# Optimization experiments

Hardware: AMD Instinct MI355X
Metric: run time of the kernel (lower is better)

## Reference

```python
import jax, jax.numpy as jnp
import numpy as np

EPSILON = 0.1
ALPHA = 0.5
N_ITER = 10
B, N, D, N_USERS = 4096, 4096, 16, 100000


def setup_inputs() -> dict:
    key = jax.random.key(0)
    k1, k2, k3, k4, k5, k6 = jax.random.split(key, 6)
    users_tensor = jax.random.randint(k1, (B,), 0, N_USERS)
    pois_tensor = jax.random.randint(k2, (B, N), 0, N)
    D_tensor = jax.random.uniform(k3, (B, N), dtype=jnp.float32)
    # ScaledEmbedding: normal init scaled by 1/embedding_dim
    poi_emb = jax.random.normal(k4, (N, D), dtype=jnp.float32) / D
    user_emb = jax.random.normal(k5, (N_USERS, D), dtype=jnp.float32) / D
    capacities = jax.random.uniform(k6, (N,), dtype=jnp.float32) + 0.5
    return {"users_tensor": users_tensor, "pois_tensor": pois_tensor,
            "D_tensor": D_tensor, "poi_emb": poi_emb,
            "user_emb": user_emb, "capacities": capacities}


def reference(users_tensor, pois_tensor, D_tensor, poi_emb, user_emb, capacities):
    pe = poi_emb[pois_tensor]            # [B, N, D]
    ue = user_emb[users_tensor]          # [B, D]
    dot = jnp.einsum('bnd,bd->bn', pe, ue)   # [B, N]
    affinity = (1.0 - ALPHA) * dot - ALPHA * (D_tensor / jnp.mean(D_tensor))
    K = jnp.exp(affinity / EPSILON)      # [B, N]
    a = jnp.ones((B,), dtype=K.dtype)
    b = capacities

    def body(i, uv):
        u, v = uv
        u = a / (K @ v)        # [B]
        v = b / (K.T @ u)      # [N]
        return (u, v)

    u0 = jnp.ones((B,), dtype=K.dtype)
    v0 = jnp.ones((N,), dtype=K.dtype)
    u, v = jax.lax.fori_loop(0, N_ITER, body, (u0, v0))
    P = K * (u[:, None] * v[None, :])    # [B, N]
    return P
```

## Files before the change

### kernel.cpp

```cpp
#include <hip/hip_runtime.h>
#include <hip/hip_fp16.h>

#define BB 4096
#define NN 4096
#define RPB 4
#define RPI 16
#define IBLK (BB / RPI)
#define NSL IBLK
#define RPP 8
#define NTSLOT 60

__device__ __forceinline__ int swzK(int bid) { return (bid & 7) * 128 + (bid >> 3); }

typedef float vf4 __attribute__((ext_vector_type(4)));
typedef float vf2 __attribute__((ext_vector_type(2)));
typedef int   vi4 __attribute__((ext_vector_type(4)));
typedef float fv2 __attribute__((ext_vector_type(2)));
__device__ __forceinline__ float4 ntl4(const float4* p) {
    vf4 r = __builtin_nontemporal_load((const vf4*)p);
    return *(float4*)&r;
}
__device__ __forceinline__ int4 ntl4i(const int4* p) {
    vi4 r = __builtin_nontemporal_load((const vi4*)p);
    return *(int4*)&r;
}
__device__ __forceinline__ void nts4(float4* p, float4 v) {
    __builtin_nontemporal_store(*(vf4*)&v, (vf4*)p);
}
__device__ __forceinline__ void nts2(float2* p, float2 v) {
    __builtin_nontemporal_store(*(vf2*)&v, (vf2*)p);
}

__device__ __forceinline__ void dec4(int w, float* f) {
    fv2 lo = __builtin_amdgcn_cvt_pk_f32_fp8(w, false);
    fv2 hi = __builtin_amdgcn_cvt_pk_f32_fp8(w, true);
    f[0] = lo.x; f[1] = lo.y; f[2] = hi.x; f[3] = hi.y;
}

__global__ __launch_bounds__(256) void k_mean(
        const float* __restrict__ Dt, float* __restrict__ dsum,
        float* __restrict__ v) {
    const int tid = blockIdx.x * blockDim.x + threadIdx.x;
    const int gs = gridDim.x * blockDim.x;
    if (tid < NN) v[tid] = 1.0f;
    const float4* D4 = (const float4*)Dt;
    const int total4 = (BB * NN) / 4;
    float s = 0.f;
    for (int i = tid; i < total4; i += gs) {
        float4 d = ntl4(&D4[i]);
        s += (d.x + d.y) + (d.z + d.w);
    }
    #pragma unroll
    for (int off = 32; off > 0; off >>= 1) s += __shfl_down(s, off, 64);
    __shared__ float ls[4];
    if ((threadIdx.x & 63) == 0) ls[threadIdx.x >> 6] = s;
    __syncthreads();
    if (threadIdx.x == 0) atomicAdd(dsum, (ls[0] + ls[1]) + (ls[2] + ls[3]));
}

__global__ __launch_bounds__(256) void k_K(
        const int* __restrict__ users, const int* __restrict__ pois,
        const float* __restrict__ Dt, const float* __restrict__ poi_emb,
        const float* __restrict__ user_emb, const float* __restrict__ dsum,
        __half* __restrict__ K, unsigned char* __restrict__ K8) {
    __shared__ __half slut[RPB][NN];
    __shared__ float ues[RPB * 16];
    const int t = threadIdx.x;
    const int b0 = swzK(blockIdx.x) * RPB;
    if (t < RPB * 16) {
        int r = t >> 4, d = t & 15;
        ues[t] = user_emb[(size_t)users[b0 + r] * 16 + d];
    }
    __syncthreads();
    float ue[RPB][16];
    #pragma unroll
    for (int r = 0; r < RPB; r++)
        #pragma unroll
        for (int d = 0; d < 16; d++) ue[r][d] = ues[r * 16 + d];

    const float4* pe4 = (const float4*)poi_emb;
    for (int j = t; j < NN; j += 256) {
        float4 p0 = pe4[j * 4 + 0];
        float4 p1 = pe4[j * 4 + 1];
        float4 p2 = pe4[j * 4 + 2];
        float4 p3 = pe4[j * 4 + 3];
        #pragma unroll
        for (int r = 0; r < RPB; r++) {
            float acc = p0.x*ue[r][0]  + p0.y*ue[r][1]  + p0.z*ue[r][2]  + p0.w*ue[r][3]
                      + p1.x*ue[r][4]  + p1.y*ue[r][5]  + p1.z*ue[r][6]  + p1.w*ue[r][7]
                      + p2.x*ue[r][8]  + p2.y*ue[r][9]  + p2.z*ue[r][10] + p2.w*ue[r][11]
                      + p3.x*ue[r][12] + p3.y*ue[r][13] + p3.z*ue[r][14] + p3.w*ue[r][15];
            slut[r][j] = __float2half(acc);
        }
    }
    __syncthreads();
    const float cc = 5.0f * 16777216.0f / dsum[0];
    #pragma unroll
    for (int r = 0; r < RPB; r++) {
        const size_t base = (size_t)(b0 + r) * NN;
        const int4*   p4 = (const int4*)(pois + base);
        const float4* d4 = (const float4*)(Dt + base);
        #pragma unroll
        for (int i = 0; i < NN / 4 / 256; i++) {
            const int q = t + i * 256;
            int4   ci = ntl4i(&p4[q]);
            float4 cd = ntl4(&d4[q]);
            float k0 = __expf(5.0f * __half2float(slut[r][ci.x]) - cc * cd.x);
            float k1 = __expf(5.0f * __half2float(slut[r][ci.y]) - cc * cd.y);
            float k2 = __expf(5.0f * __half2float(slut[r][ci.z]) - cc * cd.z);
            float k3 = __expf(5.0f * __half2float(slut[r][ci.w]) - cc * cd.w);
            __half2 ha = __floats2half2_rn(k0, k1);
            __half2 hb = __floats2half2_rn(k2, k3);
            float2 w16;
            *(__half2*)&w16.x = ha;
            *(__half2*)&w16.y = hb;
            nts2((float2*)&K[base + 4 * (size_t)q], w16);
            int w8 = __builtin_amdgcn_cvt_pk_fp8_f32(16.f * k0, 16.f * k1, 0, false);
            w8 = __builtin_amdgcn_cvt_pk_fp8_f32(16.f * k2, 16.f * k3, w8, true);
            __builtin_nontemporal_store(w8, &((int*)(K8 + base))[q]);
        }
    }
}

__global__ __launch_bounds__(1024) void k_it(
        const unsigned char* __restrict__ K8, const float* __restrict__ v,
        float* __restrict__ part, float* __restrict__ u) {
    const int t = threadIdx.x;
    const int c = t & 511;
    const int rh = t >> 9;
    const int sb = (blockIdx.x & 7) * 32 + (blockIdx.x >> 3);
    const int r0 = sb * RPI + rh * 8;

    const float4* w4 = (const float4*)v;
    float4 w0 = w4[2 * c], w1 = w4[2 * c + 1];

    uint2 h8[8];
    #pragma unroll
    for (int r = 0; r < 8; r++)
        h8[r] = ((const uint2*)(K8 + (size_t)(r0 + r) * NN))[c];

    float acc[8];
    #pragma unroll
    for (int r = 0; r < 8; r++) {
        float f[8];
        dec4((int)h8[r].x, f);
        dec4((int)h8[r].y, f + 4);
        acc[r] = f[0]*w0.x + f[1]*w0.y + f[2]*w0.z + f[3]*w0.w
               + f[4]*w1.x + f[5]*w1.y + f[6]*w1.z + f[7]*w1.w;
    }
    #pragma unroll
    for (int off = 32; off > 0; off >>= 1)
        #pragma unroll
        for (int r = 0; r < 8; r++) acc[r] += __shfl_down(acc[r], off, 64);
    __shared__ float ls[16][8];
    __shared__ float us[16];
    if ((t & 63) == 0)
        #pragma unroll
        for (int r = 0; r < 8; r++) ls[t >> 6][r] = acc[r];
    __syncthreads();
    if (t < 16) {
        const int wb = (t < 8) ? 0 : 8;
        const int rr = (t < 8) ? t : (t - 8);
        float s = 0.f;
        #pragma unroll
        for (int wv = 0; wv < 8; wv++) s += ls[wb + wv][rr];
        float uu = 1.0f / s;
        us[t] = uu;
        u[sb * RPI + t] = 16.0f * uu;
    }
    __syncthreads();

    float4 A0 = make_float4(0, 0, 0, 0), A1 = A0;
    #pragma unroll
    for (int r = 0; r < 8; r++) {
        const float ur = us[rh * 8 + r];
        float f[8];
        dec4((int)h8[r].x, f);
        dec4((int)h8[r].y, f + 4);
        A0.x += ur * f[0]; A0.y += ur * f[1]; A0.z += ur * f[2]; A0.w += ur * f[3];
        A1.x += ur * f[4]; A1.y += ur * f[5]; A1.z += ur * f[6]; A1.w += ur * f[7];
    }
    __shared__ float4 ps[512][2];
    if (rh == 1) { ps[c][0] = A0; ps[c][1] = A1; }
    __syncthreads();
    if (rh == 0) {
        float4 B0 = ps[c][0], B1 = ps[c][1];
        A0.x += B0.x; A0.y += B0.y; A0.z += B0.z; A0.w += B0.w;
        A1.x += B1.x; A1.y += B1.y; A1.z += B1.z; A1.w += B1.w;
        float4* p4 = (float4*)(part + (size_t)sb * NN);
        nts4(&p4[2 * c],     A0);
        nts4(&p4[2 * c + 1], A1);
    }
}

__global__ __launch_bounds__(256) void k_red(
        const float* __restrict__ part, const float* __restrict__ cap,
        float* __restrict__ v) {
    const int t = threadIdx.x;
    const int g = blockIdx.x;
    const int j = t & 7;
    const int s = t >> 3;
    const float4* p4 = (const float4*)part;
    float4 a = make_float4(0, 0, 0, 0);
    #pragma unroll
    for (int i = 0; i < NSL / 32; i++) {
        float4 x = ntl4(&p4[(size_t)(s + 32 * i) * (NN / 4) + g * 8 + j]);
        a.x += x.x; a.y += x.y; a.z += x.z; a.w += x.w;
    }
    __shared__ float4 red[32][8];
    red[s][j] = a;
    __syncthreads();
    if (t < 8) {
        float4 b = red[0][t];
        #pragma unroll
        for (int s2 = 1; s2 < 32; s2++) {
            float4 x = red[s2][t];
            b.x += x.x; b.y += x.y; b.z += x.z; b.w += x.w;
        }
        float4 cc = ((const float4*)cap)[g * 8 + t];
        ((float4*)v)[g * 8 + t] =
            make_float4(cc.x / b.x, cc.y / b.y, cc.z / b.z, cc.w / b.w);
    }
}

__global__ __launch_bounds__(256) void k_P(
        const __half* __restrict__ K, const float* __restrict__ u,
        const float* __restrict__ v, float* __restrict__ P) {
    const int t = threadIdx.x;
    const int slot = blockIdx.x >> 3;
    const int sb = (blockIdx.x & 7) * 64 + slot;
    const int r0 = sb * RPP;
    const bool nt = (slot >= NTSLOT);
    const float4* v4 = (const float4*)v;
    float4 va0 = v4[2 * t],       va1 = v4[2 * t + 1];
    float4 vb0 = v4[512 + 2 * t], vb1 = v4[512 + 2 * t + 1];
    #pragma unroll 2
    for (int r = 0; r < RPP; r++) {
        const int b = r0 + r;
        const float ub = u[b];
        const size_t base = (size_t)b * NN;
        const float4* k4 = (const float4*)(K + base);
        float4 raw0 = nt ? ntl4(&k4[t])       : k4[t];
        float4 raw1 = nt ? ntl4(&k4[256 + t]) : k4[256 + t];
        const __half2* ha = (const __half2*)&raw0;
        const __half2* hb = (const __half2*)&raw1;
        float2 f0 = __half22float2(ha[0]);
        float2 f1 = __half22float2(ha[1]);
        float2 f2 = __half22float2(ha[2]);
        float2 f3 = __half22float2(ha[3]);
        float2 g0 = __half22float2(hb[0]);
        float2 g1 = __half22float2(hb[1]);
        float2 g2 = __half22float2(hb[2]);
        float2 g3 = __half22float2(hb[3]);
        float4* P4 = (float4*)(P + base);
        nts4(&P4[2*t],       make_float4(f0.x*ub*va0.x, f0.y*ub*va0.y, f1.x*ub*va0.z, f1.y*ub*va0.w));
        nts4(&P4[2*t+1],     make_float4(f2.x*ub*va1.x, f2.y*ub*va1.y, f3.x*ub*va1.z, f3.y*ub*va1.w));
        nts4(&P4[512+2*t],   make_float4(g0.x*ub*vb0.x, g0.y*ub*vb0.y, g1.x*ub*vb0.z, g1.y*ub*vb0.w));
        nts4(&P4[512+2*t+1], make_float4(g2.x*ub*vb1.x, g2.y*ub*vb1.y, g3.x*ub*vb1.z, g3.y*ub*vb1.w));
    }
}

extern "C" void kernel_launch(void* const* d_in, const int* in_sizes, int n_in,
                              void* d_out, int out_size, void* d_ws, size_t ws_size,
                              hipStream_t stream) {
    const int*   users    = (const int*)d_in[0];
    const int*   pois     = (const int*)d_in[1];
    const float* Dt       = (const float*)d_in[2];
    const float* poi_emb  = (const float*)d_in[3];
    const float* user_emb = (const float*)d_in[4];
    const float* cap      = (const float*)d_in[5];
    float* out = (float*)d_out;

    float*  wsf  = (float*)d_ws;
    float*  dsum = wsf;
    float*  u    = wsf + 64;
    float*  v    = wsf + 64 + BB;
    __half* Kh   = (__half*)(wsf + 64 + BB + NN);
    float*  part = (float*)d_out;
    unsigned char* K8 = (unsigned char*)(part + (size_t)NSL * NN);

    (void)hipMemsetAsync(dsum, 0, sizeof(float), stream);
    k_mean<<<2048, 256, 0, stream>>>(Dt, dsum, v);
    k_K<<<BB / RPB, 256, 0, stream>>>(users, pois, Dt, poi_emb, user_emb, dsum, Kh, K8);
    for (int it = 0; it < 10; it++) {
        k_it<<<IBLK, 1024, 0, stream>>>(K8, v, part, u);
        k_red<<<128, 256, 0, stream>>>(part, cap, v);
    }
    k_P<<<BB / RPP, 256, 0, stream>>>(Kh, u, v, out);
}
```

Baseline: 358.4 us.

## Fuse Sinkhorn iteration and column reduction into one kernel with counter-based grid sync

Merges the per-iteration row-scaling/partial-sum kernel and the column-reduction kernel into a single launch. Extra reducer blocks spin on per-iteration atomic counters until every producer block has published its partial column sums, then compute v. Producers publish those partials with agent-scope atomic stores. This removes one kernel launch and its boundary per iteration, ten in total. The cost is spin-waiting reducer blocks and a reliance on producer blocks being scheduled before the reducers.

```diff
diff --git a/kernel.cpp b/kernel.cpp
--- a/kernel.cpp
+++ b/kernel.cpp
@@ -5,10 +5,11 @@
 #define NN 4096
 #define RPB 4
 #define RPI 16
-#define IBLK (BB / RPI)
-#define NSL IBLK
+#define NSL 256
+#define NRED 64
 #define RPP 8
 #define NTSLOT 60
+#define CNT_INTS (10 * 8 * 16)
 
 __device__ __forceinline__ int swzK(int bid) { return (bid & 7) * 128 + (bid >> 3); }
 
@@ -37,12 +38,24 @@
     f[0] = lo.x; f[1] = lo.y; f[2] = hi.x; f[3] = hi.y;
 }
 
+__device__ __forceinline__ void ast8(unsigned long long* p, float a, float b) {
+    union { float2 f; unsigned long long q; } u;
+    u.f = make_float2(a, b);
+    __hip_atomic_store(p, u.q, __ATOMIC_RELAXED, __HIP_MEMORY_SCOPE_AGENT);
+}
+__device__ __forceinline__ float2 ald8(const unsigned long long* p) {
+    union { float2 f; unsigned long long q; } u;
+    u.q = __hip_atomic_load(p, __ATOMIC_RELAXED, __HIP_MEMORY_SCOPE_AGENT);
+    return u.f;
+}
+
 __global__ __launch_bounds__(256) void k_mean(
         const float* __restrict__ Dt, float* __restrict__ dsum,
-        float* __restrict__ v) {
+        float* __restrict__ v, int* __restrict__ cnt) {
     const int tid = blockIdx.x * blockDim.x + threadIdx.x;
     const int gs = gridDim.x * blockDim.x;
     if (tid < NN) v[tid] = 1.0f;
+    if (tid < CNT_INTS) cnt[tid] = 0;
     const float4* D4 = (const float4*)Dt;
     const int total4 = (BB * NN) / 4;
     float s = 0.f;
@@ -122,104 +135,123 @@
     }
 }
 
-__global__ __launch_bounds__(1024) void k_it(
-        const unsigned char* __restrict__ K8, const float* __restrict__ v,
-        float* __restrict__ part, float* __restrict__ u) {
+__global__ __launch_bounds__(1024) void k_itf(
+        const unsigned char* __restrict__ K8, float* __restrict__ v,
+        float* __restrict__ part, float* __restrict__ u,
+        const float* __restrict__ cap, int* __restrict__ cnt) {
     const int t = threadIdx.x;
-    const int c = t & 511;
-    const int rh = t >> 9;
-    const int sb = (blockIdx.x & 7) * 32 + (blockIdx.x >> 3);
-    const int r0 = sb * RPI + rh * 8;
-
-    const float4* w4 = (const float4*)v;
-    float4 w0 = w4[2 * c], w1 = w4[2 * c + 1];
-
-    uint2 h8[8];
-    #pragma unroll
-    for (int r = 0; r < 8; r++)
-        h8[r] = ((const uint2*)(K8 + (size_t)(r0 + r) * NN))[c];
-
-    float acc[8];
-    #pragma unroll
-    for (int r = 0; r < 8; r++) {
-        float f[8];
-        dec4((int)h8[r].x, f);
-        dec4((int)h8[r].y, f + 4);
-        acc[r] = f[0]*w0.x + f[1]*w0.y + f[2]*w0.z + f[3]*w0.w
-               + f[4]*w1.x + f[5]*w1.y + f[6]*w1.z + f[7]*w1.w;
-    }
-    #pragma unroll
-    for (int off = 32; off > 0; off >>= 1)
-        #pragma unroll
-        for (int r = 0; r < 8; r++) acc[r] += __shfl_down(acc[r], off, 64);
-    __shared__ float ls[16][8];
-    __shared__ float us[16];
-    if ((t & 63) == 0)
-        #pragma unroll
-        for (int r = 0; r < 8; r++) ls[t >> 6][r] = acc[r];
-    __syncthreads();
-    if (t < 16) {
-        const int wb = (t < 8) ? 0 : 8;
-        const int rr = (t < 8) ? t : (t - 8);
-        float s = 0.f;
-        #pragma unroll
-        for (int wv = 0; wv < 8; wv++) s += ls[wb + wv][rr];
-        float uu = 1.0f / s;
-        us[t] = uu;
-        u[sb * RPI + t] = 16.0f * uu;
-    }
-    __syncthreads();
-
-    float4 A0 = make_float4(0, 0, 0, 0), A1 = A0;
-    #pragma unroll
-    for (int r = 0; r < 8; r++) {
-        const float ur = us[rh * 8 + r];
-        float f[8];
-        dec4((int)h8[r].x, f);
-        dec4((int)h8[r].y, f + 4);
-        A0.x += ur * f[0]; A0.y += ur * f[1]; A0.z += ur * f[2]; A0.w += ur * f[3];
-        A1.x += ur * f[4]; A1.y += ur * f[5]; A1.z += ur * f[6]; A1.w += ur * f[7];
-    }
-    __shared__ float4 ps[512][2];
-    if (rh == 1) { ps[c][0] = A0; ps[c][1] = A1; }
-    __syncthreads();
-    if (rh == 0) {
-        float4 B0 = ps[c][0], B1 = ps[c][1];
-        A0.x += B0.x; A0.y += B0.y; A0.z += B0.z; A0.w += B0.w;
-        A1.x += B1.x; A1.y += B1.y; A1.z += B1.z; A1.w += B1.w;
-        float4* p4 = (float4*)(part + (size_t)sb * NN);
-        nts4(&p4[2 * c],     A0);
-        nts4(&p4[2 * c + 1], A1);
-    }
-}
-
-__global__ __launch_bounds__(256) void k_red(
-        const float* __restrict__ part, const float* __restrict__ cap,
-        float* __restrict__ v) {
-    const int t = threadIdx.x;
-    const int g = blockIdx.x;
-    const int j = t & 7;
-    const int s = t >> 3;
-    const float4* p4 = (const float4*)part;
-    float4 a = make_float4(0, 0, 0, 0);
-    #pragma unroll
-    for (int i = 0; i < NSL / 32; i++) {
-        float4 x = ntl4(&p4[(size_t)(s + 32 * i) * (NN / 4) + g * 8 + j]);
-        a.x += x.x; a.y += x.y; a.z += x.z; a.w += x.w;
-    }
-    __shared__ float4 red[32][8];
-    red[s][j] = a;
-    __syncthreads();
-    if (t < 8) {
-        float4 b = red[0][t];
-        #pragma unroll
-        for (int s2 = 1; s2 < 32; s2++) {
-            float4 x = red[s2][t];
-            b.x += x.x; b.y += x.y; b.z += x.z; b.w += x.w;
-        }
-        float4 cc = ((const float4*)cap)[g * 8 + t];
-        ((float4*)v)[g * 8 + t] =
-            make_float4(cc.x / b.x, cc.y / b.y, cc.z / b.z, cc.w / b.w);
+    if (blockIdx.x < NSL) {
+        const int c = t & 511;
+        const int rh = t >> 9;
+        const int sb = ((int)blockIdx.x & 7) * 32 + ((int)blockIdx.x >> 3);
+        const int r0 = sb * RPI + rh * 8;
+
+        const float4* w4 = (const float4*)v;
+        float4 w0 = w4[2 * c], w1 = w4[2 * c + 1];
+
+        uint2 h8[8];
+        #pragma unroll
+        for (int r = 0; r < 8; r++)
+            h8[r] = ((const uint2*)(K8 + (size_t)(r0 + r) * NN))[c];
+
+        float acc[8];
+        #pragma unroll
+        for (int r = 0; r < 8; r++) {
+            float f[8];
+            dec4((int)h8[r].x, f);
+            dec4((int)h8[r].y, f + 4);
+            acc[r] = f[0]*w0.x + f[1]*w0.y + f[2]*w0.z + f[3]*w0.w
+                   + f[4]*w1.x + f[5]*w1.y + f[6]*w1.z + f[7]*w1.w;
+        }
+        #pragma unroll
+        for (int off = 32; off > 0; off >>= 1)
+            #pragma unroll
+            for (int r = 0; r < 8; r++) acc[r] += __shfl_down(acc[r], off, 64);
+        __shared__ float ls[16][8];
+        __shared__ float us[16];
+        if ((t & 63) == 0)
+            #pragma unroll
+            for (int r = 0; r < 8; r++) ls[t >> 6][r] = acc[r];
+        __syncthreads();
+        if (t < 16) {
+            const int wb = (t < 8) ? 0 : 8;
+            const int rr = (t < 8) ? t : (t - 8);
+            float s = 0.f;
+            #pragma unroll
+            for (int wv = 0; wv < 8; wv++) s += ls[wb + wv][rr];
+            float uu = 1.0f / s;
+            us[t] = uu;
+            u[sb * RPI + t] = 16.0f * uu;
+        }
+        __syncthreads();
+
+        float4 A0 = make_float4(0, 0, 0, 0), A1 = A0;
+        #pragma unroll
+        for (int r = 0; r < 8; r++) {
+            const float ur = us[rh * 8 + r];
+            float f[8];
+            dec4((int)h8[r].x, f);
+            dec4((int)h8[r].y, f + 4);
+            A0.x += ur * f[0]; A0.y += ur * f[1]; A0.z += ur * f[2]; A0.w += ur * f[3];
+            A1.x += ur * f[4]; A1.y += ur * f[5]; A1.z += ur * f[6]; A1.w += ur * f[7];
+        }
+        __shared__ float4 ps[512][2];
+        if (rh == 1) { ps[c][0] = A0; ps[c][1] = A1; }
+        __syncthreads();
+        if (rh == 0) {
+            float4 B0 = ps[c][0], B1 = ps[c][1];
+            A0.x += B0.x; A0.y += B0.y; A0.z += B0.z; A0.w += B0.w;
+            A1.x += B1.x; A1.y += B1.y; A1.z += B1.z; A1.w += B1.w;
+            unsigned long long* pq =
+                (unsigned long long*)(part + (size_t)sb * NN) + 4 * c;
+            ast8(pq + 0, A0.x, A0.y);
+            ast8(pq + 1, A0.z, A0.w);
+            ast8(pq + 2, A1.x, A1.y);
+            ast8(pq + 3, A1.z, A1.w);
+        }
+        __syncthreads();
+        if (t == 0) {
+            asm volatile("s_waitcnt vmcnt(0)" ::: "memory");
+            __hip_atomic_fetch_add(&cnt[((int)blockIdx.x & 7) * 16], 1,
+                                   __ATOMIC_RELAXED, __HIP_MEMORY_SCOPE_AGENT);
+        }
+    } else {
+        const int rb = (int)blockIdx.x - NSL;
+        if (t == 0) {
+            int s;
+            do {
+                s = 0;
+                #pragma unroll
+                for (int x = 0; x < 8; x++)
+                    s += __hip_atomic_load(&cnt[x * 16], __ATOMIC_RELAXED,
+                                           __HIP_MEMORY_SCOPE_AGENT);
+                if (s < NSL) __builtin_amdgcn_s_sleep(16);
+            } while (s < NSL);
+        }
+        __syncthreads();
+        const int p = t & 31;
+        const int sg = t >> 5;
+        const unsigned long long* pq = (const unsigned long long*)part;
+        float a0 = 0.f, a1 = 0.f;
+        #pragma unroll
+        for (int k = 0; k < 8; k++) {
+            float2 f = ald8(&pq[(size_t)(sg + 32 * k) * (NN / 2) + 32 * rb + p]);
+            a0 += f.x; a1 += f.y;
+        }
+        __shared__ float2 rsum[32][32];
+        rsum[sg][p] = make_float2(a0, a1);
+        __syncthreads();
+        if (t < 32) {
+            float s0 = 0.f, s1 = 0.f;
+            #pragma unroll
+            for (int g = 0; g < 32; g++) {
+                float2 f = rsum[g][t];
+                s0 += f.x; s1 += f.y;
+            }
+            const int col = 64 * rb + 2 * t;
+            v[col]     = cap[col]     / s0;
+            v[col + 1] = cap[col + 1] / s1;
+        }
     }
 }
 
@@ -273,18 +305,18 @@
 
     float*  wsf  = (float*)d_ws;
     float*  dsum = wsf;
-    float*  u    = wsf + 64;
-    float*  v    = wsf + 64 + BB;
-    __half* Kh   = (__half*)(wsf + 64 + BB + NN);
+    int*    cnt  = (int*)(wsf + 64);
+    float*  u    = wsf + 64 + CNT_INTS;
+    float*  v    = u + BB;
+    __half* Kh   = (__half*)(v + NN);
     float*  part = (float*)d_out;
     unsigned char* K8 = (unsigned char*)(part + (size_t)NSL * NN);
 
     (void)hipMemsetAsync(dsum, 0, sizeof(float), stream);
-    k_mean<<<2048, 256, 0, stream>>>(Dt, dsum, v);
+    k_mean<<<2048, 256, 0, stream>>>(Dt, dsum, v, cnt);
     k_K<<<BB / RPB, 256, 0, stream>>>(users, pois, Dt, poi_emb, user_emb, dsum, Kh, K8);
     for (int it = 0; it < 10; it++) {
-        k_it<<<IBLK, 1024, 0, stream>>>(K8, v, part, u);
-        k_red<<<128, 256, 0, stream>>>(part, cap, v);
+        k_itf<<<NSL + NRED, 1024, 0, stream>>>(K8, v, part, u, cap, cnt + it * 128);
     }
     k_P<<<BB / RPP, 256, 0, stream>>>(Kh, u, v, out);
 }
```

Result: slower. 397.7 us (+11.0%).
